# Kernel optimization log

Measured on AMD Instinct MI355X. Metric: run time of the kernel, lower is better.

The kernel has to match this reference:

```python
import jax, jax.numpy as jnp
import numpy as np

N = 100000   # nodes
E = 800000   # edges
F_IN = 16
H = 64       # hidden_dim
L = 4        # num_layers
CD = 8       # contrastive_dim
BN_EPS = 1e-5


def setup_inputs() -> dict:
    key = jax.random.key(0)
    ks = jax.random.split(key, 20)
    s = 0.05
    return {
        "x": jax.random.normal(ks[0], (N, F_IN), jnp.float32),
        "edge_index": jax.random.randint(ks[1], (2, E), 0, N, jnp.int64),
        "batch": jnp.zeros((N,), jnp.int64),
        "enc_w1": jax.random.normal(ks[2], (F_IN, H), jnp.float32) * s,
        "enc_b1": jnp.zeros((H,), jnp.float32),
        "enc_w2": jax.random.normal(ks[3], (H, H), jnp.float32) * s,
        "enc_b2": jnp.zeros((H,), jnp.float32),
        "conv_w": jax.random.normal(ks[4], (L, 2 * H, H), jnp.float32) * s,
        "conv_b": jnp.zeros((L, H), jnp.float32),
        "bn_gamma": jnp.ones((L, H), jnp.float32),
        "bn_beta": jnp.zeros((L, H), jnp.float32),
        "out_w1": jax.random.normal(ks[5], (H, 64), jnp.float32) * s,
        "out_b1": jnp.zeros((64,), jnp.float32),
        "out_w2": jax.random.normal(ks[6], (64, 32), jnp.float32) * s,
        "out_b2": jnp.zeros((32,), jnp.float32),
        "out_w3": jax.random.normal(ks[7], (32, CD), jnp.float32) * s,
        "out_b3": jnp.zeros((CD,), jnp.float32),
    }


def _forward(x, edge_index, enc_w1, enc_b1, enc_w2, enc_b2,
             conv_w, conv_b, bn_gamma, bn_beta,
             out_w1, out_b1, out_w2, out_b2, out_w3, out_b3):
    row, col = edge_index[0], edge_index[1]
    # lc_encode: Linear+ELU, Linear+ELU
    h = jax.nn.elu(x @ enc_w1 + enc_b1)
    feats = jax.nn.elu(h @ enc_w2 + enc_b2)  # (N, H)

    ones = jnp.ones((E, 1), feats.dtype)
    counts = jnp.clip(jax.ops.segment_sum(ones, row, num_segments=N), 1.0)  # (N,1)
    bn_scale = 1.0 / jnp.sqrt(1.0 + BN_EPS)  # eval-mode BN: running_mean=0, running_var=1

    for i in range(L):
        xc = feats[row]               # gather centers (E, H)
        xn = feats[col]               # gather neighbors (E, H)
        ef = jnp.concatenate([xc, xn - xc], axis=-1)      # (E, 2H)
        e = jax.nn.elu(ef @ conv_w[i] + conv_b[i])        # Linear + ELU
        e = (e * bn_scale) * bn_gamma[i] + bn_beta[i]     # BatchNorm (eval); Dropout is identity
        agg = jax.ops.segment_sum(e, row, num_segments=N) / counts
        feats = agg + feats  # residual in Net.forward

    # output head (Dropout identity in eval)
    o = jax.nn.elu(feats @ out_w1 + out_b1)
    o = jax.nn.elu(o @ out_w2 + out_b2)
    return o @ out_w3 + out_b3  # (N, CD)


def reference(x, edge_index, batch, enc_w1, enc_b1, enc_w2, enc_b2,
              conv_w, conv_b, bn_gamma, bn_beta,
              out_w1, out_b1, out_w2, out_b2, out_w3, out_b3):
    out = _forward(x, edge_index, enc_w1, enc_b1, enc_w2, enc_b2,
                   conv_w, conv_b, bn_gamma, bn_beta,
                   out_w1, out_b1, out_w2, out_b2, out_w3, out_b3)
    return (out, batch)
```

## Files before the change

### kernel.cpp

```cpp
#include <hip/hip_runtime.h>

#define NN 100000
#define NE 800000
#define FIN 16
#define H 64
#define NL 4
#define CDIM 8
#define NT 1563
#define NABF 1563
#define NGB 6250
#define NGH 12500
#define ROWS_PER_OWN 12500
#define ECHUNK 2048
#define NCHUNK ((NE + ECHUNK - 1) / ECHUNK)
#define NSC (NCHUNK * 8)
#define CAP 32
#define HOT 8
#define SPILL (CAP - HOT)

typedef __attribute__((ext_vector_type(8))) short bf16x8;
typedef __attribute__((ext_vector_type(4))) float f32x4;

__device__ __forceinline__ float elu(float x) { return x > 0.f ? x : __expf(x) - 1.f; }
__device__ __forceinline__ float4 elu4(float4 v) {
    return make_float4(elu(v.x), elu(v.y), elu(v.z), elu(v.w));
}

__device__ __forceinline__ unsigned short f2bf(float x) {
    union { float f; unsigned int u; } v; v.f = x;
    unsigned int r = v.u + 0x7fffu + ((v.u >> 16) & 1u);
    return (unsigned short)(r >> 16);
}
__device__ __forceinline__ float u2f(unsigned int u) {
    union { unsigned int u; float f; } v; v.u = u;
    return v.f;
}

__global__ __launch_bounds__(256) void k_enc(const float* __restrict__ x,
                                             const float* __restrict__ w1,
                                             const float* __restrict__ b1,
                                             const float* __restrict__ w2,
                                             const float* __restrict__ b2,
                                             float* __restrict__ feats,
                                             int* __restrict__ cnt,
                                             const float* __restrict__ convw,
                                             unsigned short* __restrict__ WT) {
    int tid = threadIdx.x;
    if (blockIdx.x >= NT) {
        int t = (blockIdx.x - NT) * 256 + tid;
        int i = t >> 11;
        int rem = t & 2047;
        int j = rem >> 4;
        int kg = rem & 15;
        const float* W = convw + (size_t)i * 2 * H * H;
        float v[4];
#pragma unroll
        for (int q = 0; q < 4; q++) {
            int k = kg * 4 + q;
            if (j < 64) v[q] = W[k * 64 + j] - W[(64 + k) * 64 + j];
            else        v[q] = W[(64 + k) * 64 + (j - 64)];
        }
        ushort4 p;
        p.x = f2bf(v[0]); p.y = f2bf(v[1]); p.z = f2bf(v[2]); p.w = f2bf(v[3]);
        *(ushort4*)&WT[(size_t)i * 8192 + j * 64 + kg * 4] = p;
        return;
    }
    __shared__ __align__(16) float xs[64 * 16];
    __shared__ __align__(16) float w1s[16 * 64];
    __shared__ __align__(16) float ws[64 * 64];
    __shared__ __align__(16) float fs[64 * 68];
    int base = blockIdx.x * 64;
    {
        int gid = blockIdx.x * 256 + tid;
        if (gid < NN) cnt[gid] = 0;
    }
    {
        size_t ei = (size_t)base * FIN + tid * 4;
        size_t emax = (size_t)NN * FIN - 4;
        if (ei > emax) ei = emax;
        *(float4*)&xs[tid * 4] = *(const float4*)&x[ei];
    }
    ((float4*)w1s)[tid] = ((const float4*)w1)[tid];
#pragma unroll
    for (int r = 0; r < 4; r++) ((float4*)ws)[tid + 256 * r] = ((const float4*)w2)[tid + 256 * r];
    __syncthreads();

    int wave = tid >> 6, j = tid & 63;
    float bb1 = b1[j];
    for (int i = 0; i < 16; i++) {
        int nl = i * 4 + wave;
        float acc = bb1;
#pragma unroll
        for (int k = 0; k < FIN; k++) acc += xs[nl * FIN + k] * w1s[k * 64 + j];
        fs[nl * 68 + j] = elu(acc);
    }
    __syncthreads();

    int cg = tid & 15, ng = tid >> 4;
    int c0 = cg * 4;
    float4 bb = ((const float4*)b2)[cg];
    float4 acc[4];
    acc[0] = bb; acc[1] = bb; acc[2] = bb; acc[3] = bb;
#pragma unroll 2
    for (int kq = 0; kq < 16; kq++) {
        int k0 = kq * 4;
        float4 w0 = *(const float4*)&ws[(k0 + 0) * 64 + c0];
        float4 w1v = *(const float4*)&ws[(k0 + 1) * 64 + c0];
        float4 w2v = *(const float4*)&ws[(k0 + 2) * 64 + c0];
        float4 w3v = *(const float4*)&ws[(k0 + 3) * 64 + c0];
#pragma unroll
        for (int m = 0; m < 4; m++) {
            float4 f = *(const float4*)&fs[(ng * 4 + m) * 68 + k0];
            acc[m].x += f.x * w0.x + f.y * w1v.x + f.z * w2v.x + f.w * w3v.x;
            acc[m].y += f.x * w0.y + f.y * w1v.y + f.z * w2v.y + f.w * w3v.y;
            acc[m].z += f.x * w0.z + f.y * w1v.z + f.z * w2v.z + f.w * w3v.z;
            acc[m].w += f.x * w0.w + f.y * w1v.w + f.z * w2v.w + f.w * w3v.w;
        }
    }
#pragma unroll
    for (int m = 0; m < 4; m++) {
        int n = base + ng * 4 + m;
        if (n < NN) *(float4*)&feats[(size_t)n * 64 + c0] = elu4(acc[m]);
    }
}

__global__ __launch_bounds__(256, 8) void k_scab(const int* __restrict__ row,
                                                 const int* __restrict__ col,
                                                 int* cnt, int* __restrict__ hot,
                                                 int* __restrict__ spill,
                                                 const float* __restrict__ feats,
                                                 const unsigned short* __restrict__ WT,
                                                 const float* __restrict__ convb,
                                                 unsigned short* __restrict__ Am,
                                                 unsigned short* __restrict__ Bm) {
    int tid = threadIdx.x;
    if (blockIdx.x >= NABF) {
        int owner = blockIdx.x & 7;
        int chunk = (blockIdx.x - NABF) >> 3;
        int lo = owner * ROWS_PER_OWN, hi = lo + ROWS_PER_OWN;
        int base = chunk * ECHUNK;
        int end = base + ECHUNK; if (end > NE) end = NE;
        for (int e = base + tid; e < end; e += 256) {
            int r = row[e];
            if (r >= lo && r < hi) {
                int p = atomicAdd(&cnt[r], 1);
                if (p < HOT) hot[(size_t)r * HOT + p] = col[e];
                else if (p < CAP) spill[(size_t)r * SPILL + (p - HOT)] = col[e];
            }
        }
        return;
    }
    int bid = blockIdx.x;
    int wave = tid >> 6, lane = tid & 63;
    int lr = lane & 15, lk = lane >> 4;
    int nb = bid * 64 + wave * 16;
    int n = nb + lr;
    int nc = n < NN ? n : NN - 1;

    bf16x8 ff0, ff1;
    {
        float4 f0 = *(const float4*)&feats[(size_t)nc * 64 + lk * 8];
        float4 f1 = *(const float4*)&feats[(size_t)nc * 64 + lk * 8 + 4];
        float4 f2 = *(const float4*)&feats[(size_t)nc * 64 + 32 + lk * 8];
        float4 f3 = *(const float4*)&feats[(size_t)nc * 64 + 32 + lk * 8 + 4];
        ff0[0] = (short)f2bf(f0.x); ff0[1] = (short)f2bf(f0.y);
        ff0[2] = (short)f2bf(f0.z); ff0[3] = (short)f2bf(f0.w);
        ff0[4] = (short)f2bf(f1.x); ff0[5] = (short)f2bf(f1.y);
        ff0[6] = (short)f2bf(f1.z); ff0[7] = (short)f2bf(f1.w);
        ff1[0] = (short)f2bf(f2.x); ff1[1] = (short)f2bf(f2.y);
        ff1[2] = (short)f2bf(f2.z); ff1[3] = (short)f2bf(f2.w);
        ff1[4] = (short)f2bf(f3.x); ff1[5] = (short)f2bf(f3.y);
        ff1[6] = (short)f2bf(f3.z); ff1[7] = (short)f2bf(f3.w);
    }
#pragma unroll 1
    for (int ct = 0; ct < 8; ct++) {
        bf16x8 w0 = *(const bf16x8*)&WT[(ct * 16 + lr) * 64 + lk * 8];
        bf16x8 w1 = *(const bf16x8*)&WT[(ct * 16 + lr) * 64 + 32 + lk * 8];
        f32x4 acc;
        if (ct < 4) {
            float4 bq = *(const float4*)&convb[ct * 16 + lk * 4];
            acc[0] = bq.x; acc[1] = bq.y; acc[2] = bq.z; acc[3] = bq.w;
        } else {
            acc = (f32x4)(0.0f);
        }
        acc = __builtin_amdgcn_mfma_f32_16x16x32_bf16(w0, ff0, acc, 0, 0, 0);
        acc = __builtin_amdgcn_mfma_f32_16x16x32_bf16(w1, ff1, acc, 0, 0, 0);
        if (n < NN) {
            unsigned short* dst = (ct < 4) ? Am : Bm;
            int wc = (ct & 3) * 16 + lk * 4;
            ushort4 p;
            p.x = f2bf(acc[0]); p.y = f2bf(acc[1]);
            p.z = f2bf(acc[2]); p.w = f2bf(acc[3]);
            *(ushort4*)&dst[(size_t)n * 64 + wc] = p;
        }
    }
}

__global__ __launch_bounds__(256) void k_gab(const unsigned short* __restrict__ Brd,
                                             unsigned short* __restrict__ Am,
                                             unsigned short* __restrict__ Bwr,
                                             const int* __restrict__ cnt,
                                             const int* __restrict__ hot,
                                             const int* __restrict__ spill,
                                             const float* __restrict__ gamma,
                                             const float* __restrict__ beta,
                                             float* __restrict__ feats,
                                             const unsigned short* __restrict__ WT,
                                             const float* __restrict__ convb) {
    __shared__ __align__(16) unsigned short nlds[16 * 72];
    int tid = threadIdx.x;
    int wave = tid >> 6, lane = tid & 63;
    int half = lane >> 5, l = lane & 31;
    int g = l >> 3;
    int cq = l & 7, c0 = cq * 8;
    int nb16 = blockIdx.x * 16;

    const float bs = 0.99999500003749968750f;
    float4 gm0 = *(const float4*)&gamma[c0];
    float4 gm1 = *(const float4*)&gamma[c0 + 4];
    float4 bt0 = *(const float4*)&beta[c0];
    float4 bt1 = *(const float4*)&beta[c0 + 4];

#pragma unroll
    for (int t = 0; t < 2; t++) {
        int j = t * 8 + wave * 2 + half;
        int n = nb16 + j;
        int deg = cnt[n];
        if (deg > CAP) deg = CAP;
        int mycol = (l < HOT) ? hot[(size_t)n * HOT + l]
                              : spill[(size_t)n * SPILL + (l - HOT)];
        uint4 rawA = *(const uint4*)&Am[(size_t)n * H + c0];
        float4 a0 = make_float4(u2f(rawA.x << 16), u2f(rawA.x & 0xffff0000u),
                                u2f(rawA.y << 16), u2f(rawA.y & 0xffff0000u));
        float4 a1 = make_float4(u2f(rawA.z << 16), u2f(rawA.z & 0xffff0000u),
                                u2f(rawA.w << 16), u2f(rawA.w & 0xffff0000u));
        float4 f0, f1;
        if (g == 0) {
            f0 = *(const float4*)&feats[(size_t)n * H + c0];
            f1 = *(const float4*)&feats[(size_t)n * H + c0 + 4];
        }
        float4 acc0 = make_float4(0.f, 0.f, 0.f, 0.f);
        float4 acc1 = make_float4(0.f, 0.f, 0.f, 0.f);
        for (int p0 = 0; p0 < deg; p0 += 4) {
            int p = p0 + g;
            bool valid = p < deg;
            int pc = valid ? p : (deg - 1);
            int c = __shfl(mycol, (half << 5) + pc);
            uint4 raw = *(const uint4*)&Brd[(size_t)c * H + c0];
            float4 b0 = make_float4(u2f(raw.x << 16), u2f(raw.x & 0xffff0000u),
                                    u2f(raw.y << 16), u2f(raw.y & 0xffff0000u));
            float4 b1 = make_float4(u2f(raw.z << 16), u2f(raw.z & 0xffff0000u),
                                    u2f(raw.w << 16), u2f(raw.w & 0xffff0000u));
            float4 v0 = elu4(make_float4(a0.x + b0.x, a0.y + b0.y, a0.z + b0.z, a0.w + b0.w));
            float4 v1 = elu4(make_float4(a1.x + b1.x, a1.y + b1.y, a1.z + b1.z, a1.w + b1.w));
            if (valid) {
                acc0.x += v0.x; acc0.y += v0.y; acc0.z += v0.z; acc0.w += v0.w;
                acc1.x += v1.x; acc1.y += v1.y; acc1.z += v1.z; acc1.w += v1.w;
            }
        }
#pragma unroll
        for (int d = 8; d < 32; d <<= 1) {
            acc0.x += __shfl_xor(acc0.x, d); acc0.y += __shfl_xor(acc0.y, d);
            acc0.z += __shfl_xor(acc0.z, d); acc0.w += __shfl_xor(acc0.w, d);
            acc1.x += __shfl_xor(acc1.x, d); acc1.y += __shfl_xor(acc1.y, d);
            acc1.z += __shfl_xor(acc1.z, d); acc1.w += __shfl_xor(acc1.w, d);
        }
        if (g == 0) {
            if (deg > 0) {
                float inv = bs / (float)deg;
                f0.x += acc0.x * gm0.x * inv + bt0.x;
                f0.y += acc0.y * gm0.y * inv + bt0.y;
                f0.z += acc0.z * gm0.z * inv + bt0.z;
                f0.w += acc0.w * gm0.w * inv + bt0.w;
                f1.x += acc1.x * gm1.x * inv + bt1.x;
                f1.y += acc1.y * gm1.y * inv + bt1.y;
                f1.z += acc1.z * gm1.z * inv + bt1.z;
                f1.w += acc1.w * gm1.w * inv + bt1.w;
                *(float4*)&feats[(size_t)n * H + c0] = f0;
                *(float4*)&feats[(size_t)n * H + c0 + 4] = f1;
            }
            ushort4 pa, pb;
            pa.x = f2bf(f0.x); pa.y = f2bf(f0.y); pa.z = f2bf(f0.z); pa.w = f2bf(f0.w);
            pb.x = f2bf(f1.x); pb.y = f2bf(f1.y); pb.z = f2bf(f1.z); pb.w = f2bf(f1.w);
            *(ushort4*)&nlds[j * 72 + cq * 8] = pa;
            *(ushort4*)&nlds[j * 72 + cq * 8 + 4] = pb;
        }
    }
    __syncthreads();

    {
        int lr = lane & 15, lk = lane >> 4;
        bf16x8 ff[2];
#pragma unroll
        for (int kt = 0; kt < 2; kt++)
            ff[kt] = *(const bf16x8*)&nlds[lr * 72 + kt * 32 + lk * 8];
#pragma unroll
        for (int ctl = 0; ctl < 2; ctl++) {
            int ct = wave * 2 + ctl;
            bf16x8 w0 = *(const bf16x8*)&WT[(ct * 16 + lr) * 64 + lk * 8];
            bf16x8 w1 = *(const bf16x8*)&WT[(ct * 16 + lr) * 64 + 32 + lk * 8];
            f32x4 acc;
            if (ct < 4) {
                float4 bq = *(const float4*)&convb[ct * 16 + lk * 4];
                acc[0] = bq.x; acc[1] = bq.y; acc[2] = bq.z; acc[3] = bq.w;
            } else {
                acc = (f32x4)(0.0f);
            }
            acc = __builtin_amdgcn_mfma_f32_16x16x32_bf16(w0, ff[0], acc, 0, 0, 0);
            acc = __builtin_amdgcn_mfma_f32_16x16x32_bf16(w1, ff[1], acc, 0, 0, 0);
            int n = nb16 + lr;
            unsigned short* dst = (ct < 4) ? Am : Bwr;
            int wc = (ct & 3) * 16 + lk * 4;
            ushort4 p;
            p.x = f2bf(acc[0]); p.y = f2bf(acc[1]);
            p.z = f2bf(acc[2]); p.w = f2bf(acc[3]);
            *(ushort4*)&dst[(size_t)n * 64 + wc] = p;
        }
    }
}

__global__ __launch_bounds__(256) void k_ghead(const unsigned short* __restrict__ Am,
                                               const unsigned short* __restrict__ Bm,
                                               const int* __restrict__ cnt,
                                               const int* __restrict__ hot,
                                               const int* __restrict__ spill,
                                               const float* __restrict__ gamma,
                                               const float* __restrict__ beta,
                                               const float* __restrict__ feats,
                                               const float* __restrict__ w1,
                                               const float* __restrict__ b1,
                                               const float* __restrict__ w2,
                                               const float* __restrict__ b2,
                                               const float* __restrict__ w3,
                                               const float* __restrict__ b3,
                                               const int* __restrict__ batch,
                                               float* __restrict__ out,
                                               float* __restrict__ out2) {
    __shared__ __align__(16) float w1s[64 * 64];
    __shared__ __align__(16) float w2s[64 * 32];
    __shared__ __align__(16) float w3s[32 * 8];
    __shared__ __align__(16) float fs[8 * 68];
    __shared__ __align__(16) float o1s[8 * 68];
    int tid = threadIdx.x;
    int base8 = blockIdx.x * 8;

#pragma unroll
    for (int r = 0; r < 4; r++) ((float4*)w1s)[tid + 256 * r] = ((const float4*)w1)[tid + 256 * r];
    ((float4*)w2s)[tid] = ((const float4*)w2)[tid];
    ((float4*)w2s)[tid + 256] = ((const float4*)w2)[tid + 256];
    if (tid < 64) ((float4*)w3s)[tid] = ((const float4*)w3)[tid];
    if (tid < 8) out2[base8 + tid] = (float)batch[base8 + tid];

    {
        int wave = tid >> 6, lane = tid & 63;
        int half = lane >> 5, l = lane & 31;
        int j8 = wave * 2 + half;
        int n = base8 + j8;
        int g = l >> 3;
        int cq = l & 7, c0 = cq * 8;
        int deg = cnt[n];
        if (deg > CAP) deg = CAP;
        int mycol = (l < HOT) ? hot[(size_t)n * HOT + l]
                              : spill[(size_t)n * SPILL + (l - HOT)];
        uint4 rawA = *(const uint4*)&Am[(size_t)n * H + c0];
        float4 a0 = make_float4(u2f(rawA.x << 16), u2f(rawA.x & 0xffff0000u),
                                u2f(rawA.y << 16), u2f(rawA.y & 0xffff0000u));
        float4 a1 = make_float4(u2f(rawA.z << 16), u2f(rawA.z & 0xffff0000u),
                                u2f(rawA.w << 16), u2f(rawA.w & 0xffff0000u));
        float4 f0, f1;
        if (g == 0) {
            f0 = *(const float4*)&feats[(size_t)n * H + c0];
            f1 = *(const float4*)&feats[(size_t)n * H + c0 + 4];
        }
        float4 acc0 = make_float4(0.f, 0.f, 0.f, 0.f);
        float4 acc1 = make_float4(0.f, 0.f, 0.f, 0.f);
        for (int p0 = 0; p0 < deg; p0 += 4) {
            int p = p0 + g;
            bool valid = p < deg;
            int pc = valid ? p : (deg - 1);
            int c = __shfl(mycol, (half << 5) + pc);
            uint4 raw = *(const uint4*)&Bm[(size_t)c * H + c0];
            float4 b0 = make_float4(u2f(raw.x << 16), u2f(raw.x & 0xffff0000u),
                                    u2f(raw.y << 16), u2f(raw.y & 0xffff0000u));
            float4 b1 = make_float4(u2f(raw.z << 16), u2f(raw.z & 0xffff0000u),
                                    u2f(raw.w << 16), u2f(raw.w & 0xffff0000u));
            float4 v0 = elu4(make_float4(a0.x + b0.x, a0.y + b0.y, a0.z + b0.z, a0.w + b0.w));
            float4 v1 = elu4(make_float4(a1.x + b1.x, a1.y + b1.y, a1.z + b1.z, a1.w + b1.w));
            if (valid) {
                acc0.x += v0.x; acc0.y += v0.y; acc0.z += v0.z; acc0.w += v0.w;
                acc1.x += v1.x; acc1.y += v1.y; acc1.z += v1.z; acc1.w += v1.w;
            }
        }
#pragma unroll
        for (int d = 8; d < 32; d <<= 1) {
            acc0.x += __shfl_xor(acc0.x, d); acc0.y += __shfl_xor(acc0.y, d);
            acc0.z += __shfl_xor(acc0.z, d); acc0.w += __shfl_xor(acc0.w, d);
            acc1.x += __shfl_xor(acc1.x, d); acc1.y += __shfl_xor(acc1.y, d);
            acc1.z += __shfl_xor(acc1.z, d); acc1.w += __shfl_xor(acc1.w, d);
        }
        if (g == 0) {
            if (deg > 0) {
                const float bs = 0.99999500003749968750f;
                float inv = bs / (float)deg;
                float4 gm0 = *(const float4*)&gamma[c0];
                float4 gm1 = *(const float4*)&gamma[c0 + 4];
                float4 bt0 = *(const float4*)&beta[c0];
                float4 bt1 = *(const float4*)&beta[c0 + 4];
                f0.x += acc0.x * gm0.x * inv + bt0.x;
                f0.y += acc0.y * gm0.y * inv + bt0.y;
                f0.z += acc0.z * gm0.z * inv + bt0.z;
                f0.w += acc0.w * gm0.w * inv + bt0.w;
                f1.x += acc1.x * gm1.x * inv + bt1.x;
                f1.y += acc1.y * gm1.y * inv + bt1.y;
                f1.z += acc1.z * gm1.z * inv + bt1.z;
                f1.w += acc1.w * gm1.w * inv + bt1.w;
            }
            *(float4*)&fs[j8 * 68 + c0] = f0;
            *(float4*)&fs[j8 * 68 + c0 + 4] = f1;
        }
    }
    __syncthreads();

    {
        int j = tid & 63, w = tid >> 6;
        float a0 = b1[j], a1 = a0;
#pragma unroll 4
        for (int k = 0; k < 64; k++) {
            float wv = w1s[k * 64 + j];
            a0 += fs[(2 * w) * 68 + k] * wv;
            a1 += fs[(2 * w + 1) * 68 + k] * wv;
        }
        o1s[(2 * w) * 68 + j] = elu(a0);
        o1s[(2 * w + 1) * 68 + j] = elu(a1);
    }
    __syncthreads();

    float* o2s = fs;
    {
        int node = tid >> 5, j2 = tid & 31;
        float a = b2[j2];
#pragma unroll 4
        for (int k = 0; k < 64; k++) a += o1s[node * 68 + k] * w2s[k * 32 + j2];
        float r = elu(a);
        __syncthreads();
        o2s[node * 40 + j2] = r;
    }
    __syncthreads();

    if (tid < 64) {
        int node = tid >> 3, c3 = tid & 7;
        float a = b3[c3];
#pragma unroll 4
        for (int k = 0; k < 32; k++) a += o2s[node * 40 + k] * w3s[k * 8 + c3];
        out[(size_t)(base8 + node) * 8 + c3] = a;
    }
}

extern "C" void kernel_launch(void* const* d_in, const int* in_sizes, int n_in,
                              void* d_out, int out_size, void* d_ws, size_t ws_size,
                              hipStream_t stream) {
    const float* x = (const float*)d_in[0];
    const int* edge_index = (const int*)d_in[1];
    const int* batch = (const int*)d_in[2];
    const float* enc_w1 = (const float*)d_in[3];
    const float* enc_b1 = (const float*)d_in[4];
    const float* enc_w2 = (const float*)d_in[5];
    const float* enc_b2 = (const float*)d_in[6];
    const float* conv_w = (const float*)d_in[7];
    const float* conv_b = (const float*)d_in[8];
    const float* bn_gamma = (const float*)d_in[9];
    const float* bn_beta = (const float*)d_in[10];
    const float* out_w1 = (const float*)d_in[11];
    const float* out_b1 = (const float*)d_in[12];
    const float* out_w2 = (const float*)d_in[13];
    const float* out_b2 = (const float*)d_in[14];
    const float* out_w3 = (const float*)d_in[15];
    const float* out_b3 = (const float*)d_in[16];

    const int* row = edge_index;
    const int* col = edge_index + NE;

    float* feats = (float*)d_ws;
    unsigned short* Abuf = (unsigned short*)(feats + (size_t)NN * H);
    unsigned short* Bbuf0 = Abuf + (size_t)NN * H;
    unsigned short* Bbuf1 = Bbuf0 + (size_t)NN * H;
    int* cnt = (int*)(Bbuf1 + (size_t)NN * H);
    int* hot = cnt + NN;
    int* spill = hot + (size_t)NN * HOT;
    unsigned short* WT = (unsigned short*)(spill + (size_t)NN * SPILL);

    float* out = (float*)d_out;

    k_enc<<<NT + 32, 256, 0, stream>>>(x, enc_w1, enc_b1, enc_w2, enc_b2, feats, cnt,
                                       conv_w, WT);
    k_scab<<<NABF + NSC, 256, 0, stream>>>(row, col, cnt, hot, spill,
                                           feats, WT, conv_b, Abuf, Bbuf0);

    unsigned short* Brd = Bbuf0;
    unsigned short* Bwr = Bbuf1;
    for (int i = 0; i < NL - 1; i++) {
        k_gab<<<NGB, 256, 0, stream>>>(Brd, Abuf, Bwr, cnt, hot, spill,
                                       bn_gamma + (size_t)i * H, bn_beta + (size_t)i * H,
                                       feats, WT + (size_t)(i + 1) * 8192,
                                       conv_b + (size_t)(i + 1) * H);
        unsigned short* tmp = Brd; Brd = Bwr; Bwr = tmp;
    }
    k_ghead<<<NGH, 256, 0, stream>>>(Abuf, Brd, cnt, hot, spill,
                                     bn_gamma + (size_t)(NL - 1) * H,
                                     bn_beta + (size_t)(NL - 1) * H, feats,
                                     out_w1, out_b1, out_w2, out_b2, out_w3, out_b3,
                                     batch, out, out + (size_t)NN * CDIM);
}
```

Baseline: 388.1 us.

## Prefetch neighbor rows in edge gather, emit bf16 feats, slim head kernel

Edge aggregation moves into a shared helper that issues the next neighbor row load before converting and accumulating the current one, to hide gather latency. The encoder now also writes a bf16 copy of feats into a spare buffer, so the first conv kernel loads bf16 directly instead of loading fp32 and converting. The head kernel drops its 16KB shared copy of w1 in favour of global reads, gains an occupancy launch bound, loses one barrier and has its loops unrolled further. These changes trade some extra register pressure and global/L2 traffic for more latency hiding and higher occupancy.

```diff
diff --git a/kernel.cpp b/kernel.cpp
--- a/kernel.cpp
+++ b/kernel.cpp
@@ -44,7 +44,8 @@
                                              float* __restrict__ feats,
                                              int* __restrict__ cnt,
                                              const float* __restrict__ convw,
-                                             unsigned short* __restrict__ WT) {
+                                             unsigned short* __restrict__ WT,
+                                             unsigned short* __restrict__ fb16) {
     int tid = threadIdx.x;
     if (blockIdx.x >= NT) {
         int t = (blockIdx.x - NT) * 256 + tid;
@@ -96,9 +97,9 @@
     }
     __syncthreads();
 
-    int cg = tid & 15, ng = tid >> 4;
-    int c0 = cg * 4;
-    float4 bb = ((const float4*)b2)[cg];
+    int cg_ = tid & 15, ng = tid >> 4;
+    int c0 = cg_ * 4;
+    float4 bb = ((const float4*)b2)[cg_];
     float4 acc[4];
     acc[0] = bb; acc[1] = bb; acc[2] = bb; acc[3] = bb;
 #pragma unroll 2
@@ -120,7 +121,13 @@
 #pragma unroll
     for (int m = 0; m < 4; m++) {
         int n = base + ng * 4 + m;
-        if (n < NN) *(float4*)&feats[(size_t)n * 64 + c0] = elu4(acc[m]);
+        if (n < NN) {
+            float4 e = elu4(acc[m]);
+            *(float4*)&feats[(size_t)n * 64 + c0] = e;
+            ushort4 p;
+            p.x = f2bf(e.x); p.y = f2bf(e.y); p.z = f2bf(e.z); p.w = f2bf(e.w);
+            *(ushort4*)&fb16[(size_t)n * 64 + c0] = p;
+        }
     }
 }
 
@@ -128,7 +135,7 @@
                                                  const int* __restrict__ col,
                                                  int* cnt, int* __restrict__ hot,
                                                  int* __restrict__ spill,
-                                                 const float* __restrict__ feats,
+                                                 const unsigned short* __restrict__ fb16,
                                                  const unsigned short* __restrict__ WT,
                                                  const float* __restrict__ convb,
                                                  unsigned short* __restrict__ Am,
@@ -157,21 +164,8 @@
     int n = nb + lr;
     int nc = n < NN ? n : NN - 1;
 
-    bf16x8 ff0, ff1;
-    {
-        float4 f0 = *(const float4*)&feats[(size_t)nc * 64 + lk * 8];
-        float4 f1 = *(const float4*)&feats[(size_t)nc * 64 + lk * 8 + 4];
-        float4 f2 = *(const float4*)&feats[(size_t)nc * 64 + 32 + lk * 8];
-        float4 f3 = *(const float4*)&feats[(size_t)nc * 64 + 32 + lk * 8 + 4];
-        ff0[0] = (short)f2bf(f0.x); ff0[1] = (short)f2bf(f0.y);
-        ff0[2] = (short)f2bf(f0.z); ff0[3] = (short)f2bf(f0.w);
-        ff0[4] = (short)f2bf(f1.x); ff0[5] = (short)f2bf(f1.y);
-        ff0[6] = (short)f2bf(f1.z); ff0[7] = (short)f2bf(f1.w);
-        ff1[0] = (short)f2bf(f2.x); ff1[1] = (short)f2bf(f2.y);
-        ff1[2] = (short)f2bf(f2.z); ff1[3] = (short)f2bf(f2.w);
-        ff1[4] = (short)f2bf(f3.x); ff1[5] = (short)f2bf(f3.y);
-        ff1[6] = (short)f2bf(f3.z); ff1[7] = (short)f2bf(f3.w);
-    }
+    bf16x8 ff0 = *(const bf16x8*)&fb16[(size_t)nc * 64 + lk * 8];
+    bf16x8 ff1 = *(const bf16x8*)&fb16[(size_t)nc * 64 + 32 + lk * 8];
 #pragma unroll 1
     for (int ct = 0; ct < 8; ct++) {
         bf16x8 w0 = *(const bf16x8*)&WT[(ct * 16 + lr) * 64 + lk * 8];
@@ -192,6 +186,36 @@
             p.x = f2bf(acc[0]); p.y = f2bf(acc[1]);
             p.z = f2bf(acc[2]); p.w = f2bf(acc[3]);
             *(ushort4*)&dst[(size_t)n * 64 + wc] = p;
+        }
+    }
+}
+
+__device__ __forceinline__ void edge_accum(int deg, int mycol, int half, int g, int c0,
+                                           const unsigned short* __restrict__ Bsrc,
+                                           const float4& a0, const float4& a1,
+                                           float4& acc0, float4& acc1) {
+    if (deg <= 0) return;
+    int pc0 = (g < deg) ? g : (deg - 1);
+    int c = __shfl(mycol, (half << 5) + pc0);
+    uint4 raw = *(const uint4*)&Bsrc[(size_t)c * H + c0];
+    for (int p0 = 0; p0 < deg; p0 += 4) {
+        uint4 cur = raw;
+        bool valid = (p0 + g) < deg;
+        if (p0 + 4 < deg) {
+            int pn = p0 + 4 + g;
+            int pc = (pn < deg) ? pn : (deg - 1);
+            int cn = __shfl(mycol, (half << 5) + pc);
+            raw = *(const uint4*)&Bsrc[(size_t)cn * H + c0];
+        }
+        float4 b0 = make_float4(u2f(cur.x << 16), u2f(cur.x & 0xffff0000u),
+                                u2f(cur.y << 16), u2f(cur.y & 0xffff0000u));
+        float4 b1 = make_float4(u2f(cur.z << 16), u2f(cur.z & 0xffff0000u),
+                                u2f(cur.w << 16), u2f(cur.w & 0xffff0000u));
+        float4 v0 = elu4(make_float4(a0.x + b0.x, a0.y + b0.y, a0.z + b0.z, a0.w + b0.w));
+        float4 v1 = elu4(make_float4(a1.x + b1.x, a1.y + b1.y, a1.z + b1.z, a1.w + b1.w));
+        if (valid) {
+            acc0.x += v0.x; acc0.y += v0.y; acc0.z += v0.z; acc0.w += v0.w;
+            acc1.x += v1.x; acc1.y += v1.y; acc1.z += v1.z; acc1.w += v1.w;
         }
     }
 }
@@ -241,23 +265,7 @@
         }
         float4 acc0 = make_float4(0.f, 0.f, 0.f, 0.f);
         float4 acc1 = make_float4(0.f, 0.f, 0.f, 0.f);
-        for (int p0 = 0; p0 < deg; p0 += 4) {
-            int p = p0 + g;
-            bool valid = p < deg;
-            int pc = valid ? p : (deg - 1);
-            int c = __shfl(mycol, (half << 5) + pc);
-            uint4 raw = *(const uint4*)&Brd[(size_t)c * H + c0];
-            float4 b0 = make_float4(u2f(raw.x << 16), u2f(raw.x & 0xffff0000u),
-                                    u2f(raw.y << 16), u2f(raw.y & 0xffff0000u));
-            float4 b1 = make_float4(u2f(raw.z << 16), u2f(raw.z & 0xffff0000u),
-                                    u2f(raw.w << 16), u2f(raw.w & 0xffff0000u));
-            float4 v0 = elu4(make_float4(a0.x + b0.x, a0.y + b0.y, a0.z + b0.z, a0.w + b0.w));
-            float4 v1 = elu4(make_float4(a1.x + b1.x, a1.y + b1.y, a1.z + b1.z, a1.w + b1.w));
-            if (valid) {
-                acc0.x += v0.x; acc0.y += v0.y; acc0.z += v0.z; acc0.w += v0.w;
-                acc1.x += v1.x; acc1.y += v1.y; acc1.z += v1.z; acc1.w += v1.w;
-            }
-        }
+        edge_accum(deg, mycol, half, g, c0, Brd, a0, a1, acc0, acc1);
 #pragma unroll
         for (int d = 8; d < 32; d <<= 1) {
             acc0.x += __shfl_xor(acc0.x, d); acc0.y += __shfl_xor(acc0.y, d);
@@ -319,24 +327,23 @@
     }
 }
 
-__global__ __launch_bounds__(256) void k_ghead(const unsigned short* __restrict__ Am,
-                                               const unsigned short* __restrict__ Bm,
-                                               const int* __restrict__ cnt,
-                                               const int* __restrict__ hot,
-                                               const int* __restrict__ spill,
-                                               const float* __restrict__ gamma,
-                                               const float* __restrict__ beta,
-                                               const float* __restrict__ feats,
-                                               const float* __restrict__ w1,
-                                               const float* __restrict__ b1,
-                                               const float* __restrict__ w2,
-                                               const float* __restrict__ b2,
-                                               const float* __restrict__ w3,
-                                               const float* __restrict__ b3,
-                                               const int* __restrict__ batch,
-                                               float* __restrict__ out,
-                                               float* __restrict__ out2) {
-    __shared__ __align__(16) float w1s[64 * 64];
+__global__ __launch_bounds__(256, 8) void k_ghead(const unsigned short* __restrict__ Am,
+                                                  const unsigned short* __restrict__ Bm,
+                                                  const int* __restrict__ cnt,
+                                                  const int* __restrict__ hot,
+                                                  const int* __restrict__ spill,
+                                                  const float* __restrict__ gamma,
+                                                  const float* __restrict__ beta,
+                                                  const float* __restrict__ feats,
+                                                  const float* __restrict__ w1,
+                                                  const float* __restrict__ b1,
+                                                  const float* __restrict__ w2,
+                                                  const float* __restrict__ b2,
+                                                  const float* __restrict__ w3,
+                                                  const float* __restrict__ b3,
+                                                  const int* __restrict__ batch,
+                                                  float* __restrict__ out,
+                                                  float* __restrict__ out2) {
     __shared__ __align__(16) float w2s[64 * 32];
     __shared__ __align__(16) float w3s[32 * 8];
     __shared__ __align__(16) float fs[8 * 68];
@@ -344,8 +351,6 @@
     int tid = threadIdx.x;
     int base8 = blockIdx.x * 8;
 
-#pragma unroll
-    for (int r = 0; r < 4; r++) ((float4*)w1s)[tid + 256 * r] = ((const float4*)w1)[tid + 256 * r];
     ((float4*)w2s)[tid] = ((const float4*)w2)[tid];
     ((float4*)w2s)[tid + 256] = ((const float4*)w2)[tid + 256];
     if (tid < 64) ((float4*)w3s)[tid] = ((const float4*)w3)[tid];
@@ -374,23 +379,7 @@
         }
         float4 acc0 = make_float4(0.f, 0.f, 0.f, 0.f);
         float4 acc1 = make_float4(0.f, 0.f, 0.f, 0.f);
-        for (int p0 = 0; p0 < deg; p0 += 4) {
-            int p = p0 + g;
-            bool valid = p < deg;
-            int pc = valid ? p : (deg - 1);
-            int c = __shfl(mycol, (half << 5) + pc);
-            uint4 raw = *(const uint4*)&Bm[(size_t)c * H + c0];
-            float4 b0 = make_float4(u2f(raw.x << 16), u2f(raw.x & 0xffff0000u),
-                                    u2f(raw.y << 16), u2f(raw.y & 0xffff0000u));
-            float4 b1 = make_float4(u2f(raw.z << 16), u2f(raw.z & 0xffff0000u),
-                                    u2f(raw.w << 16), u2f(raw.w & 0xffff0000u));
-            float4 v0 = elu4(make_float4(a0.x + b0.x, a0.y + b0.y, a0.z + b0.z, a0.w + b0.w));
-            float4 v1 = elu4(make_float4(a1.x + b1.x, a1.y + b1.y, a1.z + b1.z, a1.w + b1.w));
-            if (valid) {
-                acc0.x += v0.x; acc0.y += v0.y; acc0.z += v0.z; acc0.w += v0.w;
-                acc1.x += v1.x; acc1.y += v1.y; acc1.z += v1.z; acc1.w += v1.w;
-            }
-        }
+        edge_accum(deg, mycol, half, g, c0, Bm, a0, a1, acc0, acc1);
 #pragma unroll
         for (int d = 8; d < 32; d <<= 1) {
             acc0.x += __shfl_xor(acc0.x, d); acc0.y += __shfl_xor(acc0.y, d);
@@ -424,9 +413,9 @@
     {
         int j = tid & 63, w = tid >> 6;
         float a0 = b1[j], a1 = a0;
-#pragma unroll 4
+#pragma unroll 8
         for (int k = 0; k < 64; k++) {
-            float wv = w1s[k * 64 + j];
+            float wv = w1[k * 64 + j];
             a0 += fs[(2 * w) * 68 + k] * wv;
             a1 += fs[(2 * w + 1) * 68 + k] * wv;
         }
@@ -439,18 +428,16 @@
     {
         int node = tid >> 5, j2 = tid & 31;
         float a = b2[j2];
-#pragma unroll 4
+#pragma unroll 8
         for (int k = 0; k < 64; k++) a += o1s[node * 68 + k] * w2s[k * 32 + j2];
-        float r = elu(a);
-        __syncthreads();
-        o2s[node * 40 + j2] = r;
+        o2s[node * 40 + j2] = elu(a);
     }
     __syncthreads();
 
     if (tid < 64) {
         int node = tid >> 3, c3 = tid & 7;
         float a = b3[c3];
-#pragma unroll 4
+#pragma unroll 8
         for (int k = 0; k < 32; k++) a += o2s[node * 40 + k] * w3s[k * 8 + c3];
         out[(size_t)(base8 + node) * 8 + c3] = a;
     }
@@ -492,9 +479,9 @@
     float* out = (float*)d_out;
 
     k_enc<<<NT + 32, 256, 0, stream>>>(x, enc_w1, enc_b1, enc_w2, enc_b2, feats, cnt,
-                                       conv_w, WT);
+                                       conv_w, WT, Bbuf1);
     k_scab<<<NABF + NSC, 256, 0, stream>>>(row, col, cnt, hot, spill,
-                                           feats, WT, conv_b, Abuf, Bbuf0);
+                                           Bbuf1, WT, conv_b, Abuf, Bbuf0);
 
     unsigned short* Brd = Bbuf0;
     unsigned short* Bwr = Bbuf1;
```

Result: faster. 362.5 us (-6.6%).
